# Kernel optimization log

Hardware: AMD Instinct MI355X
Metric: run time of the kernel (lower is better)

The kernel has to match this reference:

```python
import jax, jax.numpy as jnp
import numpy as np

EPS = 0.01
H, W = 300, 400
WORLD_SCALE = 400.0


def setup_inputs() -> dict:
    key = jax.random.key(0)
    ks = jax.random.split(key, 8)
    N, B, D, HID = 200000, 2, 256, 256
    fx = fy = 300.0
    cx, cy = W / 2.0, H / 2.0
    z = jax.random.uniform(ks[0], (N,), minval=2.0, maxval=10.0)
    u = jax.random.uniform(ks[1], (N,), minval=0.0, maxval=float(W))
    v = jax.random.uniform(ks[2], (N,), minval=0.0, maxval=float(H))
    vert_pos = jnp.stack([(u - cx) / fx * z, (v - cy) / fy * z, z], axis=0)  # [3,N]
    target_pose = jnp.tile(jnp.eye(4, dtype=jnp.float32)[None], (B, 1, 1))
    K = jnp.array([[fx, 0.0, cx], [0.0, fy, cy], [0.0, 0.0, 1.0]], dtype=jnp.float32)
    target_intrinsics = jnp.tile(K[None], (B, 1, 1))
    vert_feat = 0.1 * jax.random.normal(ks[3], (N, D), dtype=jnp.float32)
    vert_opy = jnp.ones((N,), dtype=jnp.float32)
    W1 = 0.05 * jax.random.normal(ks[4], (D + 3, HID), dtype=jnp.float32)
    b1 = jnp.zeros((HID,), dtype=jnp.float32)
    W2 = 0.05 * jax.random.normal(ks[5], (HID, 3), dtype=jnp.float32)
    b2 = jnp.zeros((3,), dtype=jnp.float32)
    bkg_col = jnp.zeros((3,), dtype=jnp.float32)
    ref_images = jax.random.normal(ks[6], (B, 3, H, W), dtype=jnp.float32)
    return {"vert_pos": vert_pos, "ref_images": ref_images, "target_pose": target_pose,
            "target_intrinsics": target_intrinsics, "vert_feat": vert_feat, "vert_opy": vert_opy,
            "W1": W1, "b1": b1, "W2": W2, "b2": b2, "bkg_col": bkg_col}


def reference(vert_pos, ref_images, target_pose, target_intrinsics,
              vert_feat, vert_opy, W1, b1, W2, b2, bkg_col):
    B = target_pose.shape[0]
    N = vert_pos.shape[1]
    # homogeneous world points, transform to target camera frame
    xyzw = jnp.concatenate([vert_pos, jnp.ones((1, N), vert_pos.dtype)], axis=0)  # [4,N]
    xyz_t = jnp.einsum('bij,jn->bin', target_pose, xyzw)[:, :3]                   # [B,3,N]
    xy_proj = jnp.einsum('bij,bjn->bin', target_intrinsics, xyz_t)                # [B,3,N]
    z = xy_proj[:, 2:3]
    eps_mask = jax.lax.stop_gradient(jnp.abs(z) < EPS)                            # [B,1,N]
    zs = jnp.where(eps_mask, EPS, z)
    uv = xy_proj[:, 0:2] / zs
    sampler = jnp.where(eps_mask, -1e6, jnp.concatenate([uv, zs], axis=1))        # [B,3,N]
    # view direction in world frame per point
    vnorm = xyz_t / jnp.linalg.norm(xyz_t, axis=1, keepdims=True)
    vh = jnp.concatenate([vnorm, jnp.zeros_like(vnorm[:, 0:1])], axis=1)          # [B,4,N]
    pose_inv = jnp.linalg.inv(target_pose)
    vdir = jnp.einsum('bij,bjn->bin', pose_inv, vh)[:, :3]                        # [B,3,N]
    vdir = vdir.transpose(0, 2, 1).reshape(B * N, 3)
    # per-point neural shading (MLP shader on concat(feat, view_dir))
    feat = jnp.broadcast_to(vert_feat[None], (B, N, vert_feat.shape[1])).reshape(B * N, -1)
    x = jnp.concatenate([feat, vdir], axis=-1)
    h = jax.nn.relu(x @ W1 + b1)
    rgb = jax.nn.sigmoid(h @ W2 + b2).reshape(B, N, 3)                            # [B,N,3]
    opacity = jnp.clip(jax.nn.sigmoid(vert_opy), 0.0, 1.0)                        # [N]
    # differentiable splat: scatter shaded colors weighted by opacity to pixels
    u_pix, v_pix, zz = sampler[:, 0], sampler[:, 1], sampler[:, 2]                # [B,N]
    ix = jnp.round(u_pix).astype(jnp.int32)
    iy = jnp.round(v_pix).astype(jnp.int32)
    valid = (ix >= 0) & (ix < W) & (iy >= 0) & (iy < H) & (zz >= 1.0)
    idx = jnp.where(valid, iy * W + ix, H * W)                                    # dump bin H*W
    wts = opacity[None, :] * valid.astype(rgb.dtype)                              # [B,N]
    seg = lambda vals, ids: jax.ops.segment_sum(vals, ids, num_segments=H * W + 1)
    num = jax.vmap(seg)(wts[..., None] * rgb, idx)[:, :H * W]                     # [B,HW,3]
    den = jax.vmap(seg)(wts, idx)[:, :H * W]                                      # [B,HW]
    fg = num / (den[..., None] + 1e-8)
    alpha = 1.0 - jnp.exp(-den)
    img = fg * alpha[..., None] + bkg_col * (1.0 - alpha[..., None])
    return img.reshape(B, H, W, 3).transpose(0, 3, 1, 2)                          # [B,3,H,W]
```

## Files before the change

### kernel.cpp

```cpp
#include <hip/hip_runtime.h>
#include <cstdint>
#include <cstddef>

#define HH 300
#define WW 400
#define HWPIX (HH*WW)

typedef __attribute__((ext_vector_type(8))) short short8_t;
typedef __attribute__((ext_vector_type(4))) float f32x4;

static __device__ __forceinline__ unsigned short f2bf(float f){
  union { float f; unsigned u; } v; v.f = f;
  unsigned r = (v.u + 0x7fffu + ((v.u >> 16) & 1u)) >> 16;
  return (unsigned short)r;
}
static __device__ __forceinline__ float bf2f(unsigned short us){
  union { unsigned u; float f; } v; v.u = ((unsigned)us) << 16;
  return v.f;
}
static __device__ __forceinline__ float dot4_x(float a0,float x0,float a1,float x1,
                                               float a2,float x2,float a3,float x3){
  #pragma clang fp contract(off)
  float s = a0*x0;
  s = s + a1*x1;
  s = s + a2*x2;
  s = s + a3*x3;
  return s;
}
static __device__ __forceinline__ float dot3_x(float a0,float x0,float a1,float x1,
                                               float a2,float x2){
  #pragma clang fp contract(off)
  float s = a0*x0;
  s = s + a1*x1;
  s = s + a2*x2;
  return s;
}

static __device__ __forceinline__ void gload_lds16(const void* g, void* l){
  __builtin_amdgcn_global_load_lds(
      (const __attribute__((address_space(1))) unsigned int*)g,
      (__attribute__((address_space(3))) unsigned int*)l, 16, 0, 0);
}

static __device__ __forceinline__ void atomAddF32(float* p, float v){
  unsafeAtomicAdd(p, v);
}

__global__ void prep_kernel(const float* __restrict__ W1, const float* __restrict__ W2,
                            const float* __restrict__ pose,
                            float* __restrict__ poseinv, unsigned short* __restrict__ W1aT,
                            float* __restrict__ ntab, int B){
  int tid = threadIdx.x;
  int bid = blockIdx.x;
  if (bid < 256){
    int k = bid, n = tid;
    int kt = k >> 6;
    int c8 = (k >> 3) & 7;
    int i  = k & 7;
    W1aT[kt*16384 + n*64 + ((c8 ^ (n & 7))<<3) + i] = f2bf(W1[k*256 + n]);
  } else {
    int n = tid;
    ntab[n*8+0] = W1[256*256 + n];
    ntab[n*8+1] = W1[257*256 + n];
    ntab[n*8+2] = W1[258*256 + n];
    ntab[n*8+3] = W2[n*3+0];
    ntab[n*8+4] = W2[n*3+1];
    ntab[n*8+5] = W2[n*3+2];
    ntab[n*8+6] = 0.f; ntab[n*8+7] = 0.f;
    if (tid < B){
      float M[4][8];
      const float* A = pose + tid*16;
      for (int i=0;i<4;i++) for (int j=0;j<4;j++){ M[i][j]=A[i*4+j]; M[i][4+j] = (i==j)?1.f:0.f; }
      for (int c=0;c<4;c++){
        int p=c;
        for (int r=c+1;r<4;r++) if (fabsf(M[r][c])>fabsf(M[p][c])) p=r;
        if (p!=c) for (int j=0;j<8;j++){ float t=M[c][j]; M[c][j]=M[p][j]; M[p][j]=t; }
        float inv = 1.f/M[c][c];
        for (int j=0;j<8;j++) M[c][j]*=inv;
        for (int r=0;r<4;r++) if (r!=c){ float f=M[r][c]; for(int j=0;j<8;j++) M[r][j]-=f*M[c][j]; }
      }
      float* O = poseinv + tid*16;
      for (int i=0;i<4;i++) for (int j=0;j<4;j++) O[i*4+j]=M[i][4+j];
    }
  }
}

__global__ __launch_bounds__(256) void mlp_scatter_kernel(
    const float* __restrict__ feat, const unsigned short* __restrict__ W1aT,
    const float* __restrict__ b1, const float* __restrict__ b2,
    const float* __restrict__ ntab,
    const float* __restrict__ vp, const float* __restrict__ opy,
    const float* __restrict__ pose, const float* __restrict__ intr,
    const float* __restrict__ poseinv,
    float* __restrict__ num, float* __restrict__ den, int N, int B)
{
  __shared__ __align__(16) char smem[40960];
  unsigned short* sA = (unsigned short*)smem;
  unsigned short* sB = (unsigned short*)(smem + 8192);
  unsigned short* sH = (unsigned short*)smem;
  float* part        = (float*)(smem + 32768);

  const int tid  = threadIdx.x;
  const int lane = tid & 63;
  const int wv   = __builtin_amdgcn_readfirstlane(tid >> 6);
  const int lr   = lane & 15;
  const int qd   = lane >> 4;
  const int m0   = blockIdx.x * 64;

  f32x4 acc[4][4];
  for (int i=0;i<4;i++) for (int j=0;j<4;j++) acc[i][j] = (f32x4){0.f,0.f,0.f,0.f};

  ushort4 uA[4];
  {
    #pragma unroll
    for (int i=0;i<4;i++){
      int q   = i*256 + tid;
      int row = q >> 4;
      int c4  = q & 15;
      long rg = m0 + row; if (rg >= N) rg = N-1;
      float4 f = *(const float4*)(feat + rg*256 + c4*4);
      ushort4 u; u.x = f2bf(f.x); u.y = f2bf(f.y); u.z = f2bf(f.z); u.w = f2bf(f.w);
      uA[i] = u;
    }
  }

  for (int kt=0; kt<4; kt++){
    #pragma unroll
    for (int i=0;i<4;i++){
      int q   = i*256 + tid;
      int row = q >> 4;
      int c4  = q & 15;
      int q8 = c4 >> 1, half = c4 & 1;
      int phys = q8 ^ (row & 7);
      *(ushort4*)(sA + row*64 + phys*8 + half*4) = uA[i];
    }
    {
      const unsigned int* gim = (const unsigned int*)(W1aT + kt*16384);
      unsigned int* lim = (unsigned int*)sB;
      #pragma unroll
      for (int i=0;i<8;i++)
        gload_lds16(gim + i*1024 + tid*4, lim + i*1024 + tid*4);
    }
    __syncthreads();

    if (kt < 3){
      #pragma unroll
      for (int i=0;i<4;i++){
        int q   = i*256 + tid;
        int row = q >> 4;
        int c4  = q & 15;
        long rg = m0 + row; if (rg >= N) rg = N-1;
        float4 f = *(const float4*)(feat + rg*256 + (kt+1)*64 + c4*4);
        ushort4 u; u.x = f2bf(f.x); u.y = f2bf(f.y); u.z = f2bf(f.z); u.w = f2bf(f.w);
        uA[i] = u;
      }
    }

    #pragma unroll
    for (int ks=0; ks<2; ks++){
      short8_t av[4], bv[4];
      int qlog = ks*4 + qd;
      #pragma unroll
      for (int mt=0; mt<4; mt++){
        int row  = mt*16 + lr;
        int phys = qlog ^ (row & 7);
        av[mt] = *(const short8_t*)(sA + row*64 + phys*8);
      }
      #pragma unroll
      for (int nt=0; nt<4; nt++){
        int n    = wv*64 + nt*16 + lr;
        int phys = qlog ^ (n & 7);
        bv[nt] = *(const short8_t*)(sB + n*64 + phys*8);
      }
      #pragma unroll
      for (int mt=0; mt<4; mt++)
        #pragma unroll
        for (int nt=0; nt<4; nt++)
          acc[mt][nt] = __builtin_amdgcn_mfma_f32_16x16x32_bf16(av[mt], bv[nt], acc[mt][nt], 0,0,0);
    }
    __syncthreads();
  }

  #pragma unroll
  for (int nt=0; nt<4; nt++){
    int n = wv*64 + nt*16 + lr;
    float bias = b1[n];
    int c = n >> 3, e = n & 7;
    #pragma unroll
    for (int mt=0; mt<4; mt++)
      #pragma unroll
      for (int rr=0; rr<4; rr++){
        int m = mt*16 + qd*4 + rr;
        sH[m*256 + ((c ^ (m & 7))<<3) + e] = f2bf(acc[mt][nt][rr] + bias);
      }
  }
  __syncthreads();

  const int r = lane;
  long vg = m0 + r;
  bool rowok = vg < N; if (!rowok) vg = N-1;
  float px = vp[vg], py = vp[(size_t)N+vg], pz = vp[2*(size_t)N+vg];
  const float* tb = ntab + (size_t)wv*64*8;
  const int rsw = r & 7;
  const unsigned short* hrow = sH + r*256;
  float opac = 1.f/(1.f+expf(-opy[vg]));

  short8_t hv[8];
  #pragma unroll
  for (int j8=0;j8<8;j8++){
    int c = wv*8 + j8;
    hv[j8] = *(const short8_t*)(hrow + ((c ^ rsw)<<3));
  }

  for (int b0=0; b0<B; b0+=2){
    int nb = (B - b0 < 2) ? (B - b0) : 2;
    float vdx0=0.f, vdy0=0.f, vdz0=0.f, sup0=-1e6f, svp0=-1e6f, szz0=-1e6f;
    float vdx1=0.f, vdy1=0.f, vdz1=0.f, sup1=-1e6f, svp1=-1e6f, szz1=-1e6f;
    #pragma unroll
    for (int bi=0; bi<2; bi++){
      if (bi < nb){
        int b = b0 + bi;
        const float* P  = pose + b*16;
        const float* Kc = intr + b*9;
        const float* Pi = poseinv + b*16;
        float xt = dot4_x(P[0],px, P[1],py, P[2], pz, P[3], 1.f);
        float yt = dot4_x(P[4],px, P[5],py, P[6], pz, P[7], 1.f);
        float zt = dot4_x(P[8],px, P[9],py, P[10],pz, P[11],1.f);
        float uu = dot3_x(Kc[0],xt, Kc[1],yt, Kc[2],zt);
        float vv = dot3_x(Kc[3],xt, Kc[4],yt, Kc[5],zt);
        float zp = dot3_x(Kc[6],xt, Kc[7],yt, Kc[8],zt);
        bool em = fabsf(zp) < 0.01f;
        float zsafe = em ? 0.01f : zp;
        float up   = em ? -1e6f : uu/zsafe;
        float vpix = em ? -1e6f : vv/zsafe;
        float zz   = em ? -1e6f : zsafe;
        float inrm = 1.f/sqrtf(xt*xt + yt*yt + zt*zt);
        float nx=xt*inrm, ny=yt*inrm, nz=zt*inrm;
        float vx = Pi[0]*nx + Pi[1]*ny + Pi[2]*nz;
        float vy = Pi[4]*nx + Pi[5]*ny + Pi[6]*nz;
        float vz = Pi[8]*nx + Pi[9]*ny + Pi[10]*nz;
        if (bi == 0){ vdx0=vx; vdy0=vy; vdz0=vz; sup0=up; svp0=vpix; szz0=zz; }
        else        { vdx1=vx; vdy1=vy; vdz1=vz; sup1=up; svp1=vpix; szz1=zz; }
      }
    }
    float a00=0.f,a01=0.f,a02=0.f, a10=0.f,a11=0.f,a12=0.f;
    #pragma unroll
    for (int j8=0;j8<8;j8++){
      #pragma unroll
      for (int e=0;e<8;e++){
        const float* t = tb + (j8*8+e)*8;
        float t0=t[0], t1=t[1], t2=t[2], t3=t[3], t4=t[4], t5=t[5];
        float hb = bf2f((unsigned short)hv[j8][e]);
        float h0 = fmaxf(hb + vdx0*t0 + vdy0*t1 + vdz0*t2, 0.f);
        float h1 = fmaxf(hb + vdx1*t0 + vdy1*t1 + vdz1*t2, 0.f);
        a00 += h0*t3; a01 += h0*t4; a02 += h0*t5;
        a10 += h1*t3; a11 += h1*t4; a12 += h1*t5;
      }
    }
    {
      int base = (wv*64 + r)*3;
      part[base+0] = a00; part[base+1] = a01; part[base+2] = a02;
      part[768+base+0] = a10; part[768+base+1] = a11; part[768+base+2] = a12;
    }
    __syncthreads();
    if ((wv & 1) < nb){
      int b = b0 + (wv & 1);
      const float* pp = part + (wv & 1)*768;
      float S_up = (wv & 1) ? sup1 : sup0;
      float S_vp = (wv & 1) ? svp1 : svp0;
      float S_zz = (wv & 1) ? szz1 : szz0;
      int ix = (int)rintf(S_up);
      int iy = (int)rintf(S_vp);
      bool valid = rowok && ix>=0 && ix<WW && iy>=0 && iy<HH && S_zz>=1.0f;
      if (valid){
        int idx = iy*WW + ix;
        if (wv < 2){
          float s0 = pp[r*3+0] + pp[(64+r)*3+0] + pp[(128+r)*3+0] + pp[(192+r)*3+0];
          float r0 = 1.f/(1.f+expf(-(s0 + b2[0])));
          atomAddF32(den + (size_t)b*HWPIX + idx, opac);
          atomAddF32(num + ((size_t)b*3+0)*HWPIX + idx, opac*r0);
        } else {
          float s1 = pp[r*3+1] + pp[(64+r)*3+1] + pp[(128+r)*3+1] + pp[(192+r)*3+1];
          float s2 = pp[r*3+2] + pp[(64+r)*3+2] + pp[(128+r)*3+2] + pp[(192+r)*3+2];
          float r1 = 1.f/(1.f+expf(-(s1 + b2[1])));
          float r2 = 1.f/(1.f+expf(-(s2 + b2[2])));
          atomAddF32(num + ((size_t)b*3+1)*HWPIX + idx, opac*r1);
          atomAddF32(num + ((size_t)b*3+2)*HWPIX + idx, opac*r2);
        }
      }
    }
    if (b0 + 2 < B) __syncthreads();
  }
}

__global__ void compose_kernel(float* __restrict__ out, const float* __restrict__ num,
                               const float* __restrict__ den,
                               const float* __restrict__ bkg, int B){
  int i = blockIdx.x*256 + threadIdx.x;
  int total = B*HWPIX;
  if (i >= total) return;
  int b = i / HWPIX;
  int pix = i - b*HWPIX;
  float d = den[i];
  float alpha = 1.f - expf(-d);
  float om = 1.f - alpha;
  float dd = d + 1e-8f;
  const float* nb_ = num + (size_t)b*3*HWPIX;
  float* ob = out + (size_t)b*3*HWPIX;
  ob[0*HWPIX + pix] = (nb_[0*HWPIX + pix]/dd)*alpha + bkg[0]*om;
  ob[1*HWPIX + pix] = (nb_[1*HWPIX + pix]/dd)*alpha + bkg[1]*om;
  ob[2*HWPIX + pix] = (nb_[2*HWPIX + pix]/dd)*alpha + bkg[2]*om;
}

extern "C" void kernel_launch(void* const* d_in, const int* in_sizes, int n_in,
                              void* d_out, int out_size, void* d_ws, size_t ws_size,
                              hipStream_t stream){
  const float* vp   = (const float*)d_in[0];
  const float* pose = (const float*)d_in[2];
  const float* intr = (const float*)d_in[3];
  const float* feat = (const float*)d_in[4];
  const float* opy  = (const float*)d_in[5];
  const float* W1   = (const float*)d_in[6];
  const float* b1   = (const float*)d_in[7];
  const float* W2   = (const float*)d_in[8];
  const float* b2   = (const float*)d_in[9];
  const float* bkg  = (const float*)d_in[10];
  float* out = (float*)d_out;
  int N = in_sizes[0]/3;
  int B = in_sizes[2]/16;

  char* ws = (char*)d_ws;
  float* poseinv        = (float*)ws;
  unsigned short* W1aT  = (unsigned short*)(ws + 256);
  float* ntab           = (float*)(ws + 256 + 131072);
  float* num            = (float*)(ws + 256 + 131072 + 8192);
  float* den            = num + (size_t)B*3*HWPIX;

  hipMemsetAsync(num, 0, (size_t)B*4*HWPIX*sizeof(float), stream);
  prep_kernel<<<257, 256, 0, stream>>>(W1, W2, pose, poseinv, W1aT, ntab, B);
  int gridM = (N + 63)/64;
  mlp_scatter_kernel<<<gridM, 256, 0, stream>>>(feat, W1aT, b1, b2, ntab, vp, opy,
                                                pose, intr, poseinv, num, den, N, B);
  compose_kernel<<<(B*HWPIX + 255)/256, 256, 0, stream>>>(out, num, den, bkg, B);
}
```

Measured before the change: 414.2 us.

## Fold accumulator zeroing into prep kernel and stage ntab table in LDS

Removes the separate hipMemsetAsync and zeroes the num/den accumulators inside prep_kernel with a grid-stride float4 loop, saving one launch. The per-neuron ntab table (8 KB) is copied into shared memory with global_load_lds at kernel start and then read as float4/float2 vector loads, replacing scalar global loads in the second-layer loop. Shared memory per block grows from 40 KB to 48 KB, which may reduce occupancy. The zero count B*HWPIX float4s covers B*4*HWPIX floats, matching the old memset size.

```diff
diff --git a/kernel.cpp b/kernel.cpp
--- a/kernel.cpp
+++ b/kernel.cpp
@@ -49,9 +49,16 @@
 __global__ void prep_kernel(const float* __restrict__ W1, const float* __restrict__ W2,
                             const float* __restrict__ pose,
                             float* __restrict__ poseinv, unsigned short* __restrict__ W1aT,
-                            float* __restrict__ ntab, int B){
+                            float* __restrict__ ntab,
+                            float* __restrict__ zbuf, int zcount4, int B){
   int tid = threadIdx.x;
   int bid = blockIdx.x;
+  {
+    float4 z = {0.f,0.f,0.f,0.f};
+    int stride = gridDim.x * blockDim.x;
+    for (int i = bid*blockDim.x + tid; i < zcount4; i += stride)
+      ((float4*)zbuf)[i] = z;
+  }
   if (bid < 256){
     int k = bid, n = tid;
     int kt = k >> 6;
@@ -94,11 +101,12 @@
     const float* __restrict__ poseinv,
     float* __restrict__ num, float* __restrict__ den, int N, int B)
 {
-  __shared__ __align__(16) char smem[40960];
+  __shared__ __align__(16) char smem[49152];
   unsigned short* sA = (unsigned short*)smem;
   unsigned short* sB = (unsigned short*)(smem + 8192);
   unsigned short* sH = (unsigned short*)smem;
   float* part        = (float*)(smem + 32768);
+  float* tlds        = (float*)(smem + 40960);
 
   const int tid  = threadIdx.x;
   const int lane = tid & 63;
@@ -106,6 +114,13 @@
   const int lr   = lane & 15;
   const int qd   = lane >> 4;
   const int m0   = blockIdx.x * 64;
+
+  {
+    const unsigned int* g = (const unsigned int*)ntab;
+    unsigned int* l = (unsigned int*)tlds;
+    gload_lds16(g + tid*4, l + tid*4);
+    gload_lds16(g + 1024 + tid*4, l + 1024 + tid*4);
+  }
 
   f32x4 acc[4][4];
   for (int i=0;i<4;i++) for (int j=0;j<4;j++) acc[i][j] = (f32x4){0.f,0.f,0.f,0.f};
@@ -200,7 +215,7 @@
   long vg = m0 + r;
   bool rowok = vg < N; if (!rowok) vg = N-1;
   float px = vp[vg], py = vp[(size_t)N+vg], pz = vp[2*(size_t)N+vg];
-  const float* tb = ntab + (size_t)wv*64*8;
+  const float* tb = tlds + (size_t)wv*64*8;
   const int rsw = r & 7;
   const unsigned short* hrow = sH + r*256;
   float opac = 1.f/(1.f+expf(-opy[vg]));
@@ -248,13 +263,14 @@
     for (int j8=0;j8<8;j8++){
       #pragma unroll
       for (int e=0;e<8;e++){
-        const float* t = tb + (j8*8+e)*8;
-        float t0=t[0], t1=t[1], t2=t[2], t3=t[3], t4=t[4], t5=t[5];
+        const float* t = tb + ((j8*8+e)<<3);
+        float4 tA = *(const float4*)(t);
+        float2 tB = *(const float2*)(t + 4);
         float hb = bf2f((unsigned short)hv[j8][e]);
-        float h0 = fmaxf(hb + vdx0*t0 + vdy0*t1 + vdz0*t2, 0.f);
-        float h1 = fmaxf(hb + vdx1*t0 + vdy1*t1 + vdz1*t2, 0.f);
-        a00 += h0*t3; a01 += h0*t4; a02 += h0*t5;
-        a10 += h1*t3; a11 += h1*t4; a12 += h1*t5;
+        float h0 = fmaxf(hb + vdx0*tA.x + vdy0*tA.y + vdz0*tA.z, 0.f);
+        float h1 = fmaxf(hb + vdx1*tA.x + vdy1*tA.y + vdz1*tA.z, 0.f);
+        a00 += h0*tA.w; a01 += h0*tB.x; a02 += h0*tB.y;
+        a10 += h1*tA.w; a11 += h1*tB.x; a12 += h1*tB.y;
       }
     }
     {
@@ -336,8 +352,8 @@
   float* num            = (float*)(ws + 256 + 131072 + 8192);
   float* den            = num + (size_t)B*3*HWPIX;
 
-  hipMemsetAsync(num, 0, (size_t)B*4*HWPIX*sizeof(float), stream);
-  prep_kernel<<<257, 256, 0, stream>>>(W1, W2, pose, poseinv, W1aT, ntab, B);
+  prep_kernel<<<257, 256, 0, stream>>>(W1, W2, pose, poseinv, W1aT, ntab,
+                                       num, B*HWPIX, B);
   int gridM = (N + 63)/64;
   mlp_scatter_kernel<<<gridM, 256, 0, stream>>>(feat, W1aT, b1, b2, ntab, vp, opy,
                                                 pose, intr, poseinv, num, den, N, B);
```

Result: no change. 408.3 us (-1.4%).
